# Optimization experiments

Measured on AMD Instinct MI355X. Metric: run time of the kernel, lower is better.

Reference implementation:

```python
import jax, jax.numpy as jnp
import numpy as np

LN_EPS = 1e-12


def setup_inputs() -> dict:
    key = jax.random.key(0)
    k1, k2, k3, k4 = jax.random.split(key, 4)
    B, H, L, D = 2, 12, 2048, 64
    q = jax.random.normal(k1, (B, H, L, D), dtype=jnp.float32)
    k = jax.random.normal(k2, (B, H, L, D), dtype=jnp.float32)
    v = jax.random.normal(k3, (B, H, L, D), dtype=jnp.float32)
    mask = jax.random.randint(k4, (1, 1, L, L), 0, 2).astype(jnp.int32)
    gamma = jnp.ones((D,), dtype=jnp.float32)
    beta = jnp.zeros((D,), dtype=jnp.float32)
    return {"q": q, "k": k, "v": v, "mask": mask, "gamma": gamma, "beta": beta}


def reference(q, k, v, mask, gamma, beta):
    # score = q @ k^T  -> [B, H, L, L]
    score = jnp.einsum("bhqd,bhkd->bhqk", q, k)
    # masked_fill(mask == 0, -10000)
    score = jnp.where(mask == 0, jnp.float32(-10000.0), score)
    # result = score @ v -> [B, H, L, D]  (no softmax)
    result = jnp.einsum("bhqk,bhkd->bhqd", score, v)
    # layer norm over the last dim (d_tensor)
    mean = jnp.mean(result, axis=-1, keepdims=True)
    var = jnp.var(result, axis=-1, keepdims=True)
    normed = (result - mean) / jnp.sqrt(var + LN_EPS)
    return normed * gamma + beta
```

## Files before the change

kernel.cpp:

```cpp
#include <hip/hip_runtime.h>

#define SEQ 2048
#define HD 64
#define NBH 24
#define TQ 64
#define TK 64
#define KROW 72
#define SROW 40

typedef __bf16 bfrag8 __attribute__((ext_vector_type(8)));
typedef __bf16 bf16x4 __attribute__((ext_vector_type(4)));
typedef float floatx4 __attribute__((ext_vector_type(4)));

__device__ __forceinline__ floatx4 mfma_16x16x32(bfrag8 a, bfrag8 b, floatx4 c) {
    return __builtin_amdgcn_mfma_f32_16x16x32_bf16(a, b, c, 0, 0, 0);
}

__global__ __launch_bounds__(256, 4)
void normattn_kernel(const float* __restrict__ qp, const float* __restrict__ kp,
                     const float* __restrict__ vp, const int* __restrict__ maskp,
                     const float* __restrict__ gammap, const float* __restrict__ betap,
                     float* __restrict__ outp)
{
    __shared__ __attribute__((aligned(16))) __bf16 sQ[TQ * KROW];
    __shared__ __attribute__((aligned(16))) __bf16 sK[TK * KROW];
    __shared__ __attribute__((aligned(16))) __bf16 sV[HD * KROW];
    __shared__ __attribute__((aligned(16))) __bf16 sS[4][16 * SROW];

    const int tid  = threadIdx.x;
    const int wave = tid >> 6;
    const int lane = tid & 63;
    const int quad = lane >> 4;
    const int l16  = lane & 15;
    const int qt   = blockIdx.x;
    const int bh   = blockIdx.y;
    const int q0   = qt * TQ;
    const int base = bh * SEQ * HD;

    {
        const floatx4* qg = (const floatx4*)(qp + base + q0 * HD);
        #pragma unroll
        for (int it = 0; it < 4; ++it) {
            int idx = tid + it * 256;
            int r = idx >> 4, c = idx & 15;
            floatx4 val = qg[idx];
            bf16x4 pk = { (__bf16)val[0], (__bf16)val[1], (__bf16)val[2], (__bf16)val[3] };
            *(bf16x4*)&sQ[r * KROW + c * 4] = pk;
        }
    }
    __syncthreads();

    bfrag8 qa0 = *(const bfrag8*)&sQ[(wave * 16 + l16) * KROW + quad * 8];
    bfrag8 qa1 = *(const bfrag8*)&sQ[(wave * 16 + l16) * KROW + quad * 8 + 32];

    floatx4 acc[4];
    #pragma unroll
    for (int i = 0; i < 4; ++i) acc[i] = (floatx4)0.0f;

    const int qrb = q0 + wave * 16 + quad * 4;

    for (int kb = 0; kb < SEQ; kb += TK) {
        __syncthreads();

        {
            const floatx4* kg = (const floatx4*)(kp + base + kb * HD);
            #pragma unroll
            for (int it = 0; it < 4; ++it) {
                int idx = tid + it * 256;
                int r = idx >> 4, c = idx & 15;
                floatx4 val = kg[idx];
                bf16x4 pk = { (__bf16)val[0], (__bf16)val[1], (__bf16)val[2], (__bf16)val[3] };
                *(bf16x4*)&sK[r * KROW + c * 4] = pk;
            }
        }
        {
            int d = tid & 63;
            #pragma unroll
            for (int it = 0; it < 4; ++it) {
                int k4 = (tid >> 6) + it * 4;
                bf16x4 pk;
                #pragma unroll
                for (int i = 0; i < 4; ++i)
                    pk[i] = (__bf16)vp[base + (kb + k4 * 4 + i) * HD + d];
                *(bf16x4*)&sV[d * KROW + k4 * 4] = pk;
            }
        }
        __syncthreads();

        #pragma unroll
        for (int kc = 0; kc < TK; kc += 32) {
            floatx4 s0 = (floatx4)0.0f, s1 = (floatx4)0.0f;
            bfrag8 b00 = *(const bfrag8*)&sK[(kc + l16) * KROW + quad * 8];
            bfrag8 b01 = *(const bfrag8*)&sK[(kc + l16) * KROW + quad * 8 + 32];
            bfrag8 b10 = *(const bfrag8*)&sK[(kc + 16 + l16) * KROW + quad * 8];
            bfrag8 b11 = *(const bfrag8*)&sK[(kc + 16 + l16) * KROW + quad * 8 + 32];
            s0 = mfma_16x16x32(qa0, b00, s0);
            s0 = mfma_16x16x32(qa1, b01, s0);
            s1 = mfma_16x16x32(qa0, b10, s1);
            s1 = mfma_16x16x32(qa1, b11, s1);

            int kbase = kb + kc + l16;
            #pragma unroll
            for (int r = 0; r < 4; ++r) {
                int mi = (qrb + r) * SEQ + kbase;
                float v0 = maskp[mi]      ? s0[r] : -10000.0f;
                float v1 = maskp[mi + 16] ? s1[r] : -10000.0f;
                sS[wave][(quad * 4 + r) * SROW + l16]      = (__bf16)v0;
                sS[wave][(quad * 4 + r) * SROW + 16 + l16] = (__bf16)v1;
            }
            asm volatile("s_waitcnt lgkmcnt(0)" ::: "memory");

            bfrag8 pa = *(const bfrag8*)&sS[wave][l16 * SROW + quad * 8];
            #pragma unroll
            for (int nt = 0; nt < 4; ++nt) {
                bfrag8 vb = *(const bfrag8*)&sV[(nt * 16 + l16) * KROW + kc + quad * 8];
                acc[nt] = mfma_16x16x32(pa, vb, acc[nt]);
            }
        }
    }

    float g[4], bt[4];
    #pragma unroll
    for (int nt = 0; nt < 4; ++nt) {
        g[nt]  = gammap[nt * 16 + l16];
        bt[nt] = betap[nt * 16 + l16];
    }
    #pragma unroll
    for (int r = 0; r < 4; ++r) {
        float s = 0.0f, s2 = 0.0f;
        #pragma unroll
        for (int nt = 0; nt < 4; ++nt) { float x = acc[nt][r]; s += x; s2 += x * x; }
        #pragma unroll
        for (int off = 1; off < 16; off <<= 1) {
            s  += __shfl_xor(s, off);
            s2 += __shfl_xor(s2, off);
        }
        float mean = s * (1.0f / 64.0f);
        float var  = s2 * (1.0f / 64.0f) - mean * mean;
        float rstd = rsqrtf(var + 1e-12f);
        int qg2 = qrb + r;
        float* orow = outp + base + qg2 * HD;
        #pragma unroll
        for (int nt = 0; nt < 4; ++nt) {
            int d = nt * 16 + l16;
            orow[d] = (acc[nt][r] - mean) * rstd * g[nt] + bt[nt];
        }
    }
}

extern "C" void kernel_launch(void* const* d_in, const int* in_sizes, int n_in,
                              void* d_out, int out_size, void* d_ws, size_t ws_size,
                              hipStream_t stream) {
    const float* q     = (const float*)d_in[0];
    const float* k     = (const float*)d_in[1];
    const float* v     = (const float*)d_in[2];
    const int*   mask  = (const int*)d_in[3];
    const float* gamma = (const float*)d_in[4];
    const float* beta  = (const float*)d_in[5];
    float* out = (float*)d_out;

    dim3 grid(SEQ / TQ, NBH);
    normattn_kernel<<<grid, 256, 0, stream>>>(q, k, v, mask, gamma, beta, out);
}
```

Measured before the change: 166.1 us.

## Pack int32 attention mask into bitmask via pre-pass and stage bits in LDS

Adds a pre-pass kernel that packs the int32 mask into a bitmask in workspace, one bit per entry. The main kernel then loads two 32-bit words per query row per key tile into shared memory instead of reading int32 mask values per element in the inner loop. If no workspace is available, it falls back to building the bits in-kernel with ballot. This cuts mask memory traffic by 32x, since the mask is reread by every head and batch, at the cost of an extra kernel launch and one more barrier-protected shared-memory buffer.

```diff
diff --git a/kernel.cpp b/kernel.cpp
--- a/kernel.cpp
+++ b/kernel.cpp
@@ -7,6 +7,8 @@
 #define TK 64
 #define KROW 72
 #define SROW 40
+#define MASK_WORDS (SEQ / 32)
+#define MASK_BITS_BYTES (SEQ * MASK_WORDS * 4)
 
 typedef __bf16 bfrag8 __attribute__((ext_vector_type(8)));
 typedef __bf16 bf16x4 __attribute__((ext_vector_type(4)));
@@ -16,9 +18,23 @@
     return __builtin_amdgcn_mfma_f32_16x16x32_bf16(a, b, c, 0, 0, 0);
 }
 
+__global__ __launch_bounds__(256)
+void mask_pack_kernel(const int* __restrict__ maskp, unsigned int* __restrict__ bits) {
+    int gid  = blockIdx.x * 256 + threadIdx.x;
+    int lane = threadIdx.x & 63;
+    unsigned long long b = __ballot(maskp[gid] != 0);
+    if (lane == 0) {
+        int w = gid >> 5;
+        bits[w]     = (unsigned int)b;
+        bits[w + 1] = (unsigned int)(b >> 32);
+    }
+}
+
+template <bool USE_WS>
 __global__ __launch_bounds__(256, 4)
 void normattn_kernel(const float* __restrict__ qp, const float* __restrict__ kp,
                      const float* __restrict__ vp, const int* __restrict__ maskp,
+                     const unsigned int* __restrict__ maskbits,
                      const float* __restrict__ gammap, const float* __restrict__ betap,
                      float* __restrict__ outp)
 {
@@ -26,6 +42,7 @@
     __shared__ __attribute__((aligned(16))) __bf16 sK[TK * KROW];
     __shared__ __attribute__((aligned(16))) __bf16 sV[HD * KROW];
     __shared__ __attribute__((aligned(16))) __bf16 sS[4][16 * SROW];
+    __shared__ __attribute__((aligned(8)))  unsigned int sMw[TQ][2];
 
     const int tid  = threadIdx.x;
     const int wave = tid >> 6;
@@ -57,7 +74,8 @@
     #pragma unroll
     for (int i = 0; i < 4; ++i) acc[i] = (floatx4)0.0f;
 
-    const int qrb = q0 + wave * 16 + quad * 4;
+    const int qrow_loc = wave * 16 + quad * 4;
+    const int qrb = q0 + qrow_loc;
 
     for (int kb = 0; kb < SEQ; kb += TK) {
         __syncthreads();
@@ -85,7 +103,28 @@
                 *(bf16x4*)&sV[d * KROW + k4 * 4] = pk;
             }
         }
+        if (USE_WS) {
+            if (tid < 128) {
+                int r = tid >> 1, w = tid & 1;
+                sMw[r][w] = maskbits[(q0 + r) * MASK_WORDS + (kb >> 5) + w];
+            }
+        } else {
+            #pragma unroll
+            for (int it = 0; it < 16; ++it) {
+                int rr = it * 4 + wave;
+                unsigned long long b = __ballot(maskp[(q0 + rr) * SEQ + kb + lane] != 0);
+                if (lane == 0) {
+                    sMw[rr][0] = (unsigned int)b;
+                    sMw[rr][1] = (unsigned int)(b >> 32);
+                }
+            }
+        }
         __syncthreads();
+
+        unsigned long long mrow[4];
+        #pragma unroll
+        for (int r = 0; r < 4; ++r)
+            mrow[r] = *(const unsigned long long*)&sMw[qrow_loc + r][0];
 
         #pragma unroll
         for (int kc = 0; kc < TK; kc += 32) {
@@ -99,12 +138,10 @@
             s1 = mfma_16x16x32(qa0, b10, s1);
             s1 = mfma_16x16x32(qa1, b11, s1);
 
-            int kbase = kb + kc + l16;
             #pragma unroll
             for (int r = 0; r < 4; ++r) {
-                int mi = (qrb + r) * SEQ + kbase;
-                float v0 = maskp[mi]      ? s0[r] : -10000.0f;
-                float v1 = maskp[mi + 16] ? s1[r] : -10000.0f;
+                float v0 = ((mrow[r] >> (kc + l16)) & 1ull)      ? s0[r] : -10000.0f;
+                float v1 = ((mrow[r] >> (kc + 16 + l16)) & 1ull) ? s1[r] : -10000.0f;
                 sS[wave][(quad * 4 + r) * SROW + l16]      = (__bf16)v0;
                 sS[wave][(quad * 4 + r) * SROW + 16 + l16] = (__bf16)v1;
             }
@@ -138,8 +175,7 @@
         float mean = s * (1.0f / 64.0f);
         float var  = s2 * (1.0f / 64.0f) - mean * mean;
         float rstd = rsqrtf(var + 1e-12f);
-        int qg2 = qrb + r;
-        float* orow = outp + base + qg2 * HD;
+        float* orow = outp + base + (qrb + r) * HD;
         #pragma unroll
         for (int nt = 0; nt < 4; ++nt) {
             int d = nt * 16 + l16;
@@ -160,5 +196,14 @@
     float* out = (float*)d_out;
 
     dim3 grid(SEQ / TQ, NBH);
-    normattn_kernel<<<grid, 256, 0, stream>>>(q, k, v, mask, gamma, beta, out);
-}
+
+    if (ws_size >= (size_t)MASK_BITS_BYTES) {
+        unsigned int* bits = (unsigned int*)d_ws;
+        mask_pack_kernel<<<SEQ * SEQ / 256, 256, 0, stream>>>(mask, bits);
+        normattn_kernel<true><<<grid, 256, 0, stream>>>(q, k, v, mask, bits,
+                                                        gamma, beta, out);
+    } else {
+        normattn_kernel<false><<<grid, 256, 0, stream>>>(q, k, v, mask, nullptr,
+                                                         gamma, beta, out);
+    }
+}
```

New measurement: 171.1 us. 3.0% more time.
